# Kernel optimization log

Hardware: AMD Instinct MI355X
Metric: run time of the kernel (lower is better)

The kernel has to match this reference:

```python
import jax, jax.numpy as jnp
import numpy as np

EPS = 1e-5
SLOPE = 0.01  # LeakyReLU negative_slope

def _ln(x, g, b):
    m = jnp.mean(x, axis=-1, keepdims=True)
    v = jnp.mean((x - m) ** 2, axis=-1, keepdims=True)
    return (x - m) * jax.lax.rsqrt(v + EPS) * g + b

def _lrelu(x):
    return jnp.where(x >= 0, x, SLOPE * x)

def _s6(x, W1, b1, W2, b2, W3, b3, A):
    # x: (B, L, D); A: (D, N). Mamba-style S6 selective scan.
    Bm = x @ W2 + b2                       # (B, L, N) input-dependent B
    Cm = x @ W3 + b3                       # (B, L, N) input-dependent C
    delta = jax.nn.softplus(x @ W1 + b1)   # (B, L, D) step sizes
    dA = jnp.exp(jnp.einsum('bld,dn->bldn', delta, A))            # (B,L,D,N)
    dBx = jnp.einsum('bld,bln->bldn', delta, Bm) * x[..., None]    # (B,L,D,N) dB * x
    Bsz, L, D = x.shape
    N = A.shape[1]
    def step(h, inp):
        dA_t, dBx_t, C_t = inp
        h = dA_t * h + dBx_t                       # (B, D, N)
        return h, jnp.einsum('bn,bdn->bd', C_t, h)  # y_t: (B, D)
    xs = (jnp.transpose(dA, (1, 0, 2, 3)),
          jnp.transpose(dBx, (1, 0, 2, 3)),
          jnp.transpose(Cm, (1, 0, 2)))
    _, ys = jax.lax.scan(step, jnp.zeros((Bsz, D, N), x.dtype), xs)
    return jnp.transpose(ys, (1, 0, 2))  # (B, L, D)

def _fwd(text, audio, video, tW1, tb1, tg1, tbe1, tW2, tb2, tg2, tbe2, sW1, sb1, sW2, sb2, sW3, sb3, sA, aW1, ab1, ag1, abe1, aW2, ab2, ag2, abe2, vW1, vb1, vg1, vbe1, vW2, vb2, vg2, vbe2, cW1, cb1, cW2, cb2):
    # text branch: Linear+LN+LeakyReLU x2, Dropout(eval=identity), S6
    t = _lrelu(_ln(text @ tW1 + tb1, tg1, tbe1))
    t = _lrelu(_ln(t @ tW2 + tb2, tg2, tbe2))
    t = _s6(t, sW1, sb1, sW2, sb2, sW3, sb3, sA)
    # audio / video branches are computed but do not feed the output (as in source)
    a = _lrelu(_ln(audio @ aW1 + ab1, ag1, abe1))
    a = _lrelu(_ln(a @ aW2 + ab2, ag2, abe2))
    v = _lrelu(_ln(video @ vW1 + vb1, vg1, vbe1))
    v = _lrelu(_ln(v @ vW2 + vb2, vg2, vbe2))
    o1 = t @ cW1 + cb1
    return o1 @ cW2 + cb2  # (B, L, 2)

def setup_inputs() -> dict:
    key = jax.random.key(0)
    ks = iter(jax.random.split(key, 64))
    def W(shape, s=0.05):
        return jax.random.normal(next(ks), shape, jnp.float32) * s
    B, L = 64, 63
    d = {
        'text': jax.random.normal(next(ks), (B, L, 100), jnp.float32),
        'audio': jax.random.normal(next(ks), (B, L, 73), jnp.float32),
        'video': jax.random.normal(next(ks), (B, L, 100), jnp.float32),
        'tW1': W((100, 128)), 'tb1': jnp.zeros(128), 'tg1': jnp.ones(128), 'tbe1': jnp.zeros(128),
        'tW2': W((128, 100)), 'tb2': jnp.zeros(100), 'tg2': jnp.ones(100), 'tbe2': jnp.zeros(100),
        'sW1': W((100, 100)), 'sb1': jnp.zeros(100),
        'sW2': W((100, 300)), 'sb2': jnp.zeros(300),
        'sW3': W((100, 300)), 'sb3': jnp.zeros(300),
        'sA': jnp.full((100, 300), 1.0 / np.sqrt(300.0), jnp.float32),  # F.normalize(ones, dim=-1)
        'aW1': W((73, 256)), 'ab1': jnp.zeros(256), 'ag1': jnp.ones(256), 'abe1': jnp.zeros(256),
        'aW2': W((256, 100)), 'ab2': jnp.zeros(100), 'ag2': jnp.ones(100), 'abe2': jnp.zeros(100),
        'vW1': W((100, 256)), 'vb1': jnp.zeros(256), 'vg1': jnp.ones(256), 'vbe1': jnp.zeros(256),
        'vW2': W((256, 100)), 'vb2': jnp.zeros(100), 'vg2': jnp.ones(100), 'vbe2': jnp.zeros(100),
        'cW1': W((100, 50)), 'cb1': jnp.zeros(50),
        'cW2': W((50, 2)), 'cb2': jnp.zeros(2),
    }
    return d

def reference(text, audio, video, tW1, tb1, tg1, tbe1, tW2, tb2, tg2, tbe2, sW1, sb1, sW2, sb2, sW3, sb3, sA, aW1, ab1, ag1, abe1, aW2, ab2, ag2, abe2, vW1, vb1, vg1, vbe1, vW2, vb2, vg2, vbe2, cW1, cb1, cW2, cb2):
    return _fwd(text, audio, video, tW1, tb1, tg1, tbe1, tW2, tb2, tg2, tbe2, sW1, sb1, sW2, sb2, sW3, sb3, sA, aW1, ab1, ag1, abe1, aW2, ab2, ag2, abe2, vW1, vb1, vg1, vbe1, vW2, vb2, vg2, vbe2, cW1, cb1, cW2, cb2)
```

## Files before the change

kernel.cpp:

```cpp
#include <hip/hip_runtime.h>
#include <hip/hip_bf16.h>


typedef __hip_bfloat16 bf16;

#define BATCH 64
#define SEQ   63
#define ROWS  (BATCH * SEQ)
#define DIN   100
#define H1    128
#define DM    100
#define NS    300

__device__ __forceinline__ float2 up2(unsigned u) {
    float2 r;
    r.x = __uint_as_float(u << 16);
    r.y = __uint_as_float(u & 0xffff0000u);
    return r;
}
template<bool ISB>
__device__ __forceinline__ float LD(const void* p, int i) {
    if (ISB) return __bfloat162float(((const bf16*)p)[i]);
    else     return ((const float*)p)[i];
}
template<bool ISB>
__device__ __forceinline__ float2 LD2(const void* p, int i) {
    if (ISB) return up2(((const unsigned*)p)[i]);
    else     return ((const float2*)p)[i];
}
__device__ __forceinline__ float waveReduceSum(float v) {
#pragma unroll
    for (int off = 32; off > 0; off >>= 1) v += __shfl_xor(v, off, 64);
    return v;
}
__device__ __forceinline__ float4 waveReduceSum4(float4 v) {
#pragma unroll
    for (int off = 32; off > 0; off >>= 1) {
        const float a = __shfl_xor(v.x, off, 64);
        const float b = __shfl_xor(v.y, off, 64);
        const float c = __shfl_xor(v.z, off, 64);
        const float d = __shfl_xor(v.w, off, 64);
        v.x += a; v.y += b; v.z += c; v.w += d;
    }
    return v;
}
__device__ __forceinline__ float lrelu(float x) { return x >= 0.f ? x : 0.01f * x; }
__device__ __forceinline__ float softplusf(float x) {
    return (x > 20.f) ? x : log1pf(__expf(x));
}
__device__ __forceinline__ bool flags_uniform(const float* __restrict__ f) {
    bool u = true;
#pragma unroll
    for (int i = 0; i < 8; ++i) u &= (f[i] > 0.5f);
    return u;
}
__device__ __forceinline__ bool detect_bf16(const unsigned short* __restrict__ probe) {
    const int l = threadIdx.x & 63;
    const unsigned u0 = probe[l * 2];
    const unsigned u1 = probe[l * 2 + 1];
    const float v0 = fabsf(__uint_as_float(u0 << 16));
    const float v1 = fabsf(__uint_as_float(u1 << 16));
    const bool big = !(v0 < 1000.f) || !(v1 < 1000.f);
    const bool zero_even = (u0 == 0u);
    const unsigned long long mb = __ballot(big);
    const unsigned long long mz = __ballot(zero_even);
    return (mb == 0ULL) && (__popcll(mz) < 32);
}

template<bool ISB>
__device__ __forceinline__ void a_main(
    const void* __restrict__ text,
    const void* __restrict__ tW1, const void* __restrict__ tb1,
    const void* __restrict__ tg1, const void* __restrict__ tbe1,
    const void* __restrict__ tW2, const void* __restrict__ tb2,
    const void* __restrict__ tg2, const void* __restrict__ tbe2,
    const void* __restrict__ sW1w, const void* __restrict__ sb1,
    float* __restrict__ ddx, float* __restrict__ t2g,
    float* __restrict__ sW,
    float (&xb)[4][DIN][2], float (&t1b)[4][H1][2], float (&t2b)[4][DM][2])
{
    const int tid  = threadIdx.x;
    const int w    = tid >> 6;
    const int lane = tid & 63;
    const int r0   = blockIdx.x * 8 + w * 2;

    if (lane < 50) {
#pragma unroll
        for (int r = 0; r < 2; ++r) {
            const float2 xv = LD2<ISB>(text, (r0 + r) * 50 + lane);
            xb[w][2 * lane][r]     = xv.x;
            xb[w][2 * lane + 1][r] = xv.y;
        }
    }
    for (int i = tid; i < 6400; i += 256)
        *(float2*)&sW[2 * i] = LD2<ISB>(tW1, i);
    __syncthreads();

    const float2 b1v = LD2<ISB>(tb1, lane);
    float ax0 = b1v.x, ay0 = b1v.y, ax1 = b1v.x, ay1 = b1v.y;
#pragma unroll 10
    for (int k = 0; k < DIN; ++k) {
        const float2 wv = *(const float2*)&sW[k * 128 + 2 * lane];
        const float2 xv = *(const float2*)&xb[w][k][0];
        ax0 += xv.x * wv.x; ay0 += xv.x * wv.y;
        ax1 += xv.y * wv.x; ay1 += xv.y * wv.y;
    }
    {
        float4 red = waveReduceSum4(make_float4(
            ax0 + ay0, ax0 * ax0 + ay0 * ay0,
            ax1 + ay1, ax1 * ax1 + ay1 * ay1));
        const float m0 = red.x * (1.f / 128.f);
        const float rs0 = rsqrtf(red.y * (1.f / 128.f) - m0 * m0 + 1e-5f);
        const float m1 = red.z * (1.f / 128.f);
        const float rs1 = rsqrtf(red.w * (1.f / 128.f) - m1 * m1 + 1e-5f);
        const float2 g = LD2<ISB>(tg1, lane), be = LD2<ISB>(tbe1, lane);
        float2 v;
        v.x = lrelu((ax0 - m0) * rs0 * g.x + be.x);
        v.y = lrelu((ax1 - m1) * rs1 * g.x + be.x);
        *(float2*)&t1b[w][2 * lane][0] = v;
        v.x = lrelu((ay0 - m0) * rs0 * g.y + be.y);
        v.y = lrelu((ay1 - m1) * rs1 * g.y + be.y);
        *(float2*)&t1b[w][2 * lane + 1][0] = v;
    }
    __syncthreads();

    for (int i = tid; i < 6400; i += 256)
        *(float2*)&sW[2 * i] = LD2<ISB>(tW2, i);
    __syncthreads();

    const bool act = lane < 50;
    const int  li  = act ? lane : 0;
    const float2 b2v = LD2<ISB>(tb2, li);
    float cx0 = b2v.x, cy0 = b2v.y, cx1 = b2v.x, cy1 = b2v.y;
#pragma unroll 8
    for (int k = 0; k < H1; ++k) {
        const float2 wv = *(const float2*)&sW[k * 100 + 2 * li];
        const float2 tv = *(const float2*)&t1b[w][k][0];
        cx0 += tv.x * wv.x; cy0 += tv.x * wv.y;
        cx1 += tv.y * wv.x; cy1 += tv.y * wv.y;
    }
    float u0x, u0y, u1x, u1y;
    {
        float4 red = waveReduceSum4(act ? make_float4(
            cx0 + cy0, cx0 * cx0 + cy0 * cy0,
            cx1 + cy1, cx1 * cx1 + cy1 * cy1) : make_float4(0.f, 0.f, 0.f, 0.f));
        const float m0 = red.x * 0.01f;
        const float rs0 = rsqrtf(red.y * 0.01f - m0 * m0 + 1e-5f);
        const float m1 = red.z * 0.01f;
        const float rs1 = rsqrtf(red.w * 0.01f - m1 * m1 + 1e-5f);
        if (act) {
            const float2 g = LD2<ISB>(tg2, lane), be = LD2<ISB>(tbe2, lane);
            u0x = lrelu((cx0 - m0) * rs0 * g.x + be.x);
            u0y = lrelu((cy0 - m0) * rs0 * g.y + be.y);
            u1x = lrelu((cx1 - m1) * rs1 * g.x + be.x);
            u1y = lrelu((cy1 - m1) * rs1 * g.y + be.y);
            t2b[w][2 * lane][0] = u0x; t2b[w][2 * lane + 1][0] = u0y;
            t2b[w][2 * lane][1] = u1x; t2b[w][2 * lane + 1][1] = u1y;
            *(float2*)(t2g + (r0)     * DM + 2 * lane) = make_float2(u0x, u0y);
            *(float2*)(t2g + (r0 + 1) * DM + 2 * lane) = make_float2(u1x, u1y);
        }
    }
    __syncthreads();

    for (int i = tid; i < 5000; i += 256)
        *(float2*)&sW[2 * i] = LD2<ISB>(sW1w, i);
    __syncthreads();

    const float2 sbv = LD2<ISB>(sb1, li);
    float dA0x = sbv.x, dA0y = sbv.y, dA1x = sbv.x, dA1y = sbv.y;
#pragma unroll 10
    for (int k = 0; k < DM; ++k) {
        const float2 wv = *(const float2*)&sW[k * 100 + 2 * li];
        const float2 tv = *(const float2*)&t2b[w][k][0];
        dA0x += tv.x * wv.x; dA0y += tv.x * wv.y;
        dA1x += tv.y * wv.x; dA1y += tv.y * wv.y;
    }
    if (act) {
        float de0 = softplusf(dA0x), de1 = softplusf(dA0y);
        float4 o;
        o.x = de0; o.y = de0 * u0x; o.z = de1; o.w = de1 * u0y;
        *(float4*)(ddx + (r0) * (2 * DM) + 4 * lane) = o;
        de0 = softplusf(dA1x); de1 = softplusf(dA1y);
        o.x = de0; o.y = de0 * u1x; o.z = de1; o.w = de1 * u1y;
        *(float4*)(ddx + (r0 + 1) * (2 * DM) + 4 * lane) = o;
    }
}

template<bool ISB>
__device__ __forceinline__ void a_prep(
    const void* __restrict__ sW2, const void* __restrict__ sb2,
    const void* __restrict__ sW3, const void* __restrict__ sb3,
    float* __restrict__ M33p, float* __restrict__ k0w, float* __restrict__ sW,
    int d3)
{
    const int tid = threadIdx.x;
    const int w = tid >> 6, lane = tid & 63;
    float* W3row = sW;
    float* b2v   = sW + 320;
    float* b3v   = sW + 640;
    for (int i = tid; i < 300; i += 256) {
        W3row[i] = LD<ISB>(sW3, d3 * 300 + i);
        b2v[i]   = LD<ISB>(sb2, i);
        b3v[i]   = LD<ISB>(sb3, i);
    }
    __syncthreads();
    for (int g = 0; g < 6; ++g) {
        const int d2 = w * 25 + g * 4;
        float4 p = make_float4(0.f, 0.f, 0.f, 0.f);
#pragma unroll
        for (int rep = 0; rep < 5; ++rep) {
            const int n = lane + 64 * rep;
            if (n < 300) {
                const float w3 = W3row[n];
                p.x += LD<ISB>(sW2, (d2 + 0) * 300 + n) * w3;
                p.y += LD<ISB>(sW2, (d2 + 1) * 300 + n) * w3;
                p.z += LD<ISB>(sW2, (d2 + 2) * 300 + n) * w3;
                p.w += LD<ISB>(sW2, (d2 + 3) * 300 + n) * w3;
            }
        }
        p = waveReduceSum4(p);
        if (lane == 0) {
            M33p[d3 * 102 + d2 + 0] = p.x;
            M33p[d3 * 102 + d2 + 1] = p.y;
            M33p[d3 * 102 + d2 + 2] = p.z;
            M33p[d3 * 102 + d2 + 3] = p.w;
        }
    }
    {
        const int d2 = w * 25 + 24;
        float4 p = make_float4(0.f, 0.f, 0.f, 0.f);
#pragma unroll
        for (int rep = 0; rep < 5; ++rep) {
            const int n = lane + 64 * rep;
            if (n < 300) {
                p.x += LD<ISB>(sW2, d2 * 300 + n) * W3row[n];
                if (w == 0) p.y += W3row[n] * b2v[n];
                if (w == 1) p.y += LD<ISB>(sW2, d3 * 300 + n) * b3v[n];
                if (w == 2 && d3 == 0) p.y += b2v[n] * b3v[n];
            }
        }
        p = waveReduceSum4(p);
        if (lane == 0) {
            M33p[d3 * 102 + d2] = p.x;
            if (w == 0) M33p[d3 * 102 + 100] = p.y;
            if (w == 1) M33p[d3 * 102 + 101] = p.y;
            if (w == 2 && d3 == 0) k0w[0] = p.y;
        }
    }
}

template<bool ISB>
__device__ __forceinline__ void a_check(
    const void* __restrict__ sA, float* __restrict__ Afl,
    float* __restrict__ sW, int j)
{
    const int tid = threadIdx.x;
    const float a0 = LD<ISB>(sA, 0);
    bool ok = true;
    for (int i = j * 3750 + tid; i < (j + 1) * 3750; i += 256)
        ok &= (LD<ISB>(sA, i) == a0);
    if (tid == 0) sW[960] = 1.f;
    __syncthreads();
    if (!ok) sW[960] = 0.f;
    __syncthreads();
    if (tid == 0) Afl[j] = sW[960];
    if (j == 0 && tid == 1) Afl[8] = a0;
}

template<bool ISB>
__device__ __forceinline__ void a_mkv(
    const void* __restrict__ cW1, const void* __restrict__ cb1,
    const void* __restrict__ cW2, const void* __restrict__ cb2,
    float* __restrict__ Mkv)
{
    const int t = threadIdx.x;
    if (t < 200) {
        const int d = t >> 1, j = t & 1;
        float m = 0.f;
#pragma unroll 5
        for (int i = 0; i < 50; ++i)
            m += LD<ISB>(cW1, d * 50 + i) * LD<ISB>(cW2, 2 * i + j);
        Mkv[t] = m;
    } else if (t < 202) {
        const int j = t - 200;
        float kv = LD<ISB>(cb2, j);
#pragma unroll 5
        for (int i = 0; i < 50; ++i)
            kv += LD<ISB>(cb1, i) * LD<ISB>(cW2, 2 * i + j);
        Mkv[200 + j] = kv;
    }
}

__global__ __launch_bounds__(256) void k_A(
    const void* text,
    const void* tW1, const void* tb1, const void* tg1, const void* tbe1,
    const void* tW2, const void* tb2, const void* tg2, const void* tbe2,
    const void* sW1w, const void* sb1,
    const void* sW2, const void* sb2, const void* sW3, const void* sb3,
    const void* sA,
    const void* cW1, const void* cb1, const void* cW2, const void* cb2,
    float* ddx, float* t2g, float* Mkv, float* M33p, float* k0w, float* Afl,
    const unsigned short* probe)
{
    __shared__ __align__(16) float sW[12800];
    __shared__ __align__(16) float xb[4][DIN][2];
    __shared__ __align__(16) float t1b[4][H1][2];
    __shared__ __align__(16) float t2b[4][DM][2];
    const bool isb = detect_bf16(probe);
    const int blk = blockIdx.x;
    if (blk < 504) {
        if (isb) a_main<true >(text, tW1, tb1, tg1, tbe1, tW2, tb2, tg2, tbe2,
                               sW1w, sb1, ddx, t2g, sW, xb, t1b, t2b);
        else     a_main<false>(text, tW1, tb1, tg1, tbe1, tW2, tb2, tg2, tbe2,
                               sW1w, sb1, ddx, t2g, sW, xb, t1b, t2b);
    } else if (blk < 604) {
        if (isb) a_prep<true >(sW2, sb2, sW3, sb3, M33p, k0w, sW, blk - 504);
        else     a_prep<false>(sW2, sb2, sW3, sb3, M33p, k0w, sW, blk - 504);
    } else if (blk < 612) {
        if (isb) a_check<true >(sA, Afl, sW, blk - 604);
        else     a_check<false>(sA, Afl, sW, blk - 604);
    } else {
        if (isb) a_mkv<true >(cW1, cb1, cW2, cb2, Mkv);
        else     a_mkv<false>(cW1, cb1, cW2, cb2, Mkv);
    }
}

template<bool ISB>
__device__ __forceinline__ void gyh_impl(
    const float* __restrict__ t2g, const float* __restrict__ ddx,
    const float* __restrict__ M33p, const float* __restrict__ k0w,
    const float* __restrict__ Mkv, const float* __restrict__ Afl,
    void* __restrict__ outp,
    float* __restrict__ sT2, float* __restrict__ sM,
    float* __restrict__ sZ, float* __restrict__ sG,
    float* __restrict__ srv, float* __restrict__ sMk)
{
    const int bid = blockIdx.x;
    const int xcd = bid & 7;
    const int jj  = bid >> 3;
    const int b   = xcd * 8 + (jj >> 2);
    const int q   = jj & 3;
    const int tid = threadIdx.x;
    const int w = tid >> 6, lane = tid & 63;

    const int tmax  = (q * 16 + 15 < SEQ) ? q * 16 + 15 : SEQ - 1;
    const int srows = tmax + 1;

    float2 rdd[13];
#pragma unroll
    for (int j = 0; j < 13; ++j) {
        const int i = tid + j * 512;
        rdd[j] = (i < srows * 100) ? ((const float2*)ddx)[b * 6300 + i]
                                   : make_float2(0.f, 0.f);
    }

    for (int i = tid; i < srows * 50; i += 512) {
        const float2 v = ((const float2*)t2g)[b * 3150 + i];
        const int t = i / 50, k2 = i % 50;
        sT2[t * 102 + 2 * k2]     = v.x;
        sT2[t * 102 + 2 * k2 + 1] = v.y;
    }
    for (int i = tid; i < 5100; i += 512)
        *(float2*)&sM[2 * i] = ((const float2*)M33p)[i];
    if (tid < 202) sMk[tid] = Mkv[tid];
    __syncthreads();

    {
        const float mv0 = sM[lane * 102 + 101];
        const float mv1 = (lane < 36) ? sM[(64 + lane) * 102 + 101] : 0.f;
#pragma unroll
        for (int g = 0; g < 2; ++g) {
            float4 p;
            float acc[4];
#pragma unroll
            for (int i = 0; i < 4; ++i) {
                const int s = w * 8 + g * 4 + i;
                const int scl = (s <= tmax) ? s : 0;
                float a = sT2[scl * 102 + lane] * mv0;
                if (lane < 36) a += sT2[scl * 102 + 64 + lane] * mv1;
                acc[i] = a;
            }
            p = waveReduceSum4(make_float4(acc[0], acc[1], acc[2], acc[3]));
            if (lane == 0) {
                const int s0 = w * 8 + g * 4;
                srv[s0 + 0] = p.x; srv[s0 + 1] = p.y;
                srv[s0 + 2] = p.z; srv[s0 + 3] = p.w;
            }
        }
    }
    {
        const int l2 = (lane < 51) ? 2 * lane : 0;
        const int zr0 = w * 2, zr1 = w * 2 + 1;
        const int t0 = q * 16 + zr0;
        const int t1 = q * 16 + zr1;
        const int tc1 = (t1 <= tmax) ? t1 : tmax;
        float2 a0 = make_float2(0.f, 0.f);
        float2 a1 = make_float2(0.f, 0.f);
#pragma unroll 4
        for (int k = 0; k < 100; ++k) {
            const float2 wv = *(const float2*)&sM[k * 102 + l2];
            const float x0 = sT2[t0 * 102 + k];
            const float x1 = sT2[tc1 * 102 + k];
            a0.x += x0 * wv.x; a0.y += x0 * wv.y;
            a1.x += x1 * wv.x; a1.y += x1 * wv.y;
        }
        if (lane < 51) {
            *(float2*)&sZ[zr0 * 102 + l2] = a0;
            if (t1 <= tmax) *(float2*)&sZ[zr1 * 102 + l2] = a1;
        }
    }
    __syncthreads();

    {
        const float kz = k0w[0];
        const int sc  = (lane <= tmax) ? lane : tmax;
        const int zr0 = w * 2, zr1 = w * 2 + 1;
        const int t1  = q * 16 + zr1;
        float g0 = kz + sZ[zr0 * 102 + 100] + srv[sc];
        float g1 = kz + sZ[zr1 * 102 + 100] + srv[sc];
#pragma unroll 5
        for (int k2 = 0; k2 < 50; ++k2) {
            const float2 tv = *(const float2*)&sT2[sc * 102 + 2 * k2];
            const float2 z0 = *(const float2*)&sZ[zr0 * 102 + 2 * k2];
            const float2 z1 = *(const float2*)&sZ[zr1 * 102 + 2 * k2];
            g0 += z0.x * tv.x + z0.y * tv.y;
            g1 += z1.x * tv.x + z1.y * tv.y;
        }
        if (lane <= tmax) {
            sG[zr0 * 64 + lane] = g0;
            if (t1 <= tmax) sG[zr1 * 64 + lane] = g1;
        }
    }
    __syncthreads();

#pragma unroll
    for (int j = 0; j < 13; ++j) {
        const int i = tid + j * 512;
        if (i < srows * 100) {
            sT2[i] = rdd[j].x;
            sM[i]  = rdd[j].y;
        }
    }
    __syncthreads();

    {
        const float av = Afl[8];
        const int c = tid >> 7;
        const int d = tid & 127;
        const int L = (srows + 3) >> 2;
        const int s0 = c * L;
        const int s1 = (s0 + L < srows) ? s0 + L : srows;
        if (d < 100) {
            float Ts = 0.f;
            for (int s = s0; s < s1; ++s) Ts += sT2[s * 100 + d];
            sZ[c * 128 + d] = Ts;
        }
        __syncthreads();
        if (d < 100) {
            float D = 0.f;
            for (int cc = 0; cc < c; ++cc) D += sZ[cc * 128 + d];
            for (int s = s0; s < s1; ++s) {
                D += sT2[s * 100 + d];
                const float En = __expf(-av * D);
                sM[s * 100 + d] = sM[s * 100 + d] * En;
                const int zr = s - q * 16;
                if (zr >= 0) sM[6400 + zr * 100 + d] = __expf(av * D);
            }
        }
    }
    __syncthreads();

    {
        const int li = (lane < 50) ? lane : 49;
        const float4 mk = *(const float4*)&sMk[4 * li];
        float4 oc = make_float4(0.f, 0.f, 0.f, 0.f);
#pragma unroll
        for (int r = 0; r < 2; ++r) {
            const int zr = w * 2 + r;
            const int t  = q * 16 + zr;
            float o0 = 0.f, o1 = 0.f;
            if (t < SEQ) {
                float a0 = 0.f, a1 = 0.f;
                const int nf = (t + 1) >> 1;
                const float* gp = &sG[zr * 64];
                for (int s2 = 0; s2 < nf; ++s2) {
                    const float2 g2 = *(const float2*)&gp[2 * s2];
                    const float2 v0 = *(const float2*)&sM[(2 * s2) * 100 + 2 * li];
                    const float2 v1 = *(const float2*)&sM[(2 * s2 + 1) * 100 + 2 * li];
                    a0 += g2.x * v0.x + g2.y * v1.x;
                    a1 += g2.x * v0.y + g2.y * v1.y;
                }
                if ((t & 1) == 0) {
                    const float gg = gp[t];
                    const float2 vt = *(const float2*)&sM[t * 100 + 2 * li];
                    a0 += gg * vt.x; a1 += gg * vt.y;
                }
                const float2 e2 = *(const float2*)&sM[6400 + zr * 100 + 2 * li];
                const float y0 = (lane < 50) ? e2.x * a0 : 0.f;
                const float y1 = (lane < 50) ? e2.y * a1 : 0.f;
                o0 = y0 * mk.x + y1 * mk.z;
                o1 = y0 * mk.y + y1 * mk.w;
            }
            if (r == 0) { oc.x = o0; oc.y = o1; }
            else        { oc.z = o0; oc.w = o1; }
        }
        oc = waveReduceSum4(oc);
        if (lane == 0) {
            const float kv0 = sMk[200], kv1 = sMk[201];
#pragma unroll
            for (int r = 0; r < 2; ++r) {
                const int t = q * 16 + w * 2 + r;
                if (t >= SEQ) continue;
                const int row = b * SEQ + t;
                const float o0 = (r == 0 ? oc.x : oc.z) + kv0;
                const float o1 = (r == 0 ? oc.y : oc.w) + kv1;
                if (ISB) {
                    ((bf16*)outp)[row * 2 + 0] = __float2bfloat16(o0);
                    ((bf16*)outp)[row * 2 + 1] = __float2bfloat16(o1);
                } else {
                    *(float2*)((float*)outp + row * 2) = make_float2(o0, o1);
                }
            }
        }
    }
}

__global__ __launch_bounds__(512) void k_GYH(
    const float* __restrict__ t2g, const float* __restrict__ ddx,
    const float* __restrict__ M33p, const float* __restrict__ k0w,
    const float* __restrict__ Mkv, const float* __restrict__ Afl,
    void* __restrict__ outp, const unsigned short* __restrict__ probe)
{
    __shared__ __align__(16) float sT2[6426];
    __shared__ __align__(16) float sM[10240];
    __shared__ __align__(16) float sZ[1632];
    __shared__ __align__(16) float sG[1024];
    __shared__ __align__(16) float srv[64];
    __shared__ __align__(16) float sMk[204];
    if (!flags_uniform(Afl)) return;
    if (detect_bf16(probe))
        gyh_impl<true >(t2g, ddx, M33p, k0w, Mkv, Afl, outp, sT2, sM, sZ, sG, srv, sMk);
    else
        gyh_impl<false>(t2g, ddx, M33p, k0w, Mkv, Afl, outp, sT2, sM, sZ, sG, srv, sMk);
}

template<bool ISB>
__device__ __forceinline__ float4 LD4(const void* p, int i) {
    if (ISB) {
        const uint2 u = ((const uint2*)p)[i];
        float4 r;
        r.x = __uint_as_float(u.x << 16);
        r.y = __uint_as_float(u.x & 0xffff0000u);
        r.z = __uint_as_float(u.y << 16);
        r.w = __uint_as_float(u.y & 0xffff0000u);
        return r;
    } else return ((const float4*)p)[i];
}

template<bool ISB>
__device__ __forceinline__ void b_impl(
    const float* __restrict__ t2g,
    const void* __restrict__ sW2, const void* __restrict__ sb2,
    const void* __restrict__ sW3, const void* __restrict__ sb3,
    float* __restrict__ BC, float (&sT)[DM][8])
{
    const int t  = threadIdx.x;
    const int r0 = blockIdx.x * 8;
    if (t < DM) {
#pragma unroll
        for (int r = 0; r < 8; ++r) sT[t][r] = t2g[(r0 + r) * DM + t];
    }
    __syncthreads();
    const bool isB = t < 75;
    const bool valid = t < 150;
    const int colbase = isB ? 4 * t : (valid ? 4 * (t - 75) : 0);
    const void* Wp   = isB ? sW2 : sW3;
    const void* bias = isB ? sb2 : sb3;
    const int rs4 = NS >> 2;
    const int cb4 = colbase >> 2;
    float4 acc[8];
    {
        const float4 bv = LD4<ISB>(bias, cb4);
#pragma unroll
        for (int r = 0; r < 8; ++r) acc[r] = bv;
    }
    float4 ring[4];
#pragma unroll
    for (int j = 0; j < 4; ++j) ring[j] = LD4<ISB>(Wp, j * rs4 + cb4);
    for (int kk = 0; kk < DM; kk += 4) {
#pragma unroll
        for (int j = 0; j < 4; ++j) {
            const int k = kk + j;
            const float4 wv = ring[j];
            if (k + 4 < DM) ring[j] = LD4<ISB>(Wp, (k + 4) * rs4 + cb4);
            const float4 lo = *(const float4*)&sT[k][0];
            const float4 hi = *(const float4*)&sT[k][4];
            acc[0].x += lo.x * wv.x; acc[0].y += lo.x * wv.y; acc[0].z += lo.x * wv.z; acc[0].w += lo.x * wv.w;
            acc[1].x += lo.y * wv.x; acc[1].y += lo.y * wv.y; acc[1].z += lo.y * wv.z; acc[1].w += lo.y * wv.w;
            acc[2].x += lo.z * wv.x; acc[2].y += lo.z * wv.y; acc[2].z += lo.z * wv.z; acc[2].w += lo.z * wv.w;
            acc[3].x += lo.w * wv.x; acc[3].y += lo.w * wv.y; acc[3].z += lo.w * wv.z; acc[3].w += lo.w * wv.w;
            acc[4].x += hi.x * wv.x; acc[4].y += hi.x * wv.y; acc[4].z += hi.x * wv.z; acc[4].w += hi.x * wv.w;
            acc[5].x += hi.y * wv.x; acc[5].y += hi.y * wv.y; acc[5].z += hi.y * wv.z; acc[5].w += hi.y * wv.w;
            acc[6].x += hi.z * wv.x; acc[6].y += hi.z * wv.y; acc[6].z += hi.z * wv.z; acc[6].w += hi.z * wv.w;
            acc[7].x += hi.w * wv.x; acc[7].y += hi.w * wv.y; acc[7].z += hi.w * wv.z; acc[7].w += hi.w * wv.w;
        }
    }
    if (valid) {
        const int off = isB ? 0 : 1;
#pragma unroll
        for (int r = 0; r < 8; ++r) {
            float* bp = BC + (r0 + r) * (2 * NS) + 2 * colbase + off;
            bp[0] = acc[r].x; bp[2] = acc[r].y;
            bp[4] = acc[r].z; bp[6] = acc[r].w;
        }
    }
}

__global__ __launch_bounds__(192, 1) void k_B(
    const float* t2g, const void* sW2, const void* sb2,
    const void* sW3, const void* sb3, float* BC,
    const float* Afl, const unsigned short* probe)
{
    __shared__ __align__(16) float sT[DM][8];
    if (flags_uniform(Afl)) return;
    if (detect_bf16(probe)) b_impl<true >(t2g, sW2, sb2, sW3, sb3, BC, sT);
    else                    b_impl<false>(t2g, sW2, sb2, sW3, sb3, BC, sT);
}

template<bool ISB>
__device__ __forceinline__ void scan_impl(
    const float* __restrict__ ddx, const float* __restrict__ BC,
    const void* __restrict__ sA, float* __restrict__ y,
    float (&sacc)[4][16][2][68])
{
    const int w    = threadIdx.x >> 6;
    const int lane = threadIdx.x & 63;
    const int wid  = blockIdx.x * 4 + w;
    const int b    = wid / 50;
    const int dp   = wid % 50;
    const int d0   = 2 * dp, d1 = d0 + 1;

    int nc[5]; bool nv[5];
    float A0[5], A1[5], h0[5], h1[5];
#pragma unroll
    for (int c = 0; c < 5; ++c) {
        const int n = lane + 64 * c;
        nv[c] = n < NS;
        nc[c] = nv[c] ? n : 0;
        A0[c] = nv[c] ? LD<ISB>(sA, d0 * NS + nc[c]) : 0.f;
        A1[c] = nv[c] ? LD<ISB>(sA, d1 * NS + nc[c]) : 0.f;
        h0[c] = 0.f; h1[c] = 0.f;
    }
    const float* ddp = ddx + (b * SEQ) * (2 * DM) + 4 * dp;
    const float* BCp = BC  + (b * SEQ) * (2 * NS);
    float*       yp  = y   + (b * SEQ) * DM + d0;

    float4 pdd[3];
    float2 pbc[3][5];
#pragma unroll
    for (int j = 0; j < 3; ++j) {
        pdd[j] = *(const float4*)(ddp + j * (2 * DM));
#pragma unroll
        for (int c = 0; c < 5; ++c)
            pbc[j][c] = nv[c] ? *(const float2*)(BCp + j * (2 * NS) + 2 * nc[c])
                              : make_float2(0.f, 0.f);
    }
    const int pr = lane >> 1;
    const int hh = lane & 1;
    const int sa = pr & 15;
    const int aa = pr >> 4;

#pragma unroll 3
    for (int l = 0; l < SEQ; ++l) {
        const int bi = l % 3;
        const float4 dd = pdd[bi];
        float2 bc[5];
#pragma unroll
        for (int c = 0; c < 5; ++c) bc[c] = pbc[bi][c];
        if (l + 3 < SEQ) {
            pdd[bi] = *(const float4*)(ddp + (l + 3) * (2 * DM));
#pragma unroll
            for (int c = 0; c < 5; ++c)
                pbc[bi][c] = nv[c] ? *(const float2*)(BCp + (l + 3) * (2 * NS) + 2 * nc[c])
                                   : make_float2(0.f, 0.f);
        }
        float a0 = 0.f, a1 = 0.f;
#pragma unroll
        for (int c = 0; c < 5; ++c) {
            h0[c] = __expf(dd.x * A0[c]) * h0[c] + dd.y * bc[c].x;
            a0 += bc[c].y * h0[c];
            h1[c] = __expf(dd.z * A1[c]) * h1[c] + dd.w * bc[c].x;
            a1 += bc[c].y * h1[c];
        }
        const int s = l & 15;
        sacc[w][s][0][lane] = a0;
        sacc[w][s][1][lane] = a1;

        if (s == 15 || l == SEQ - 1) {
            const int l0 = l & ~15;
            const int cs = l - l0 + 1;
            float sum = 0.f;
            if (sa < cs) {
                const float* rowp = &sacc[w][sa][aa][hh * 32];
#pragma unroll
                for (int i = 0; i < 8; ++i) {
                    const float4 v = *(const float4*)(rowp + 4 * i);
                    sum += v.x + v.y + v.z + v.w;
                }
            }
            sum += __shfl_xor(sum, 1, 64);
            if (hh == 0 && sa < cs) yp[(l0 + sa) * DM + aa] = sum;
        }
    }
}

__global__ __launch_bounds__(256) void k_scan(
    const float* ddx, const float* BC, const void* sA, float* y,
    const float* Afl, const unsigned short* probe)
{
    __shared__ __align__(16) float sacc[4][16][2][68];
    if (flags_uniform(Afl)) return;
    if (detect_bf16(probe)) scan_impl<true >(ddx, BC, sA, y, sacc);
    else                    scan_impl<false>(ddx, BC, sA, y, sacc);
}

template<bool ISB>
__device__ __forceinline__ void headf_impl(
    const float* __restrict__ y, const float* __restrict__ Mkv,
    void* __restrict__ outp)
{
    const int row = blockIdx.x * 256 + threadIdx.x;
    if (row >= ROWS) return;
    float a0 = Mkv[200], a1 = Mkv[201];
    const float* yr = y + row * DM;
#pragma unroll 4
    for (int k = 0; k < DM; ++k) {
        const float v = yr[k];
        const float2 m = *(const float2*)(Mkv + 2 * k);
        a0 += v * m.x;
        a1 += v * m.y;
    }
    if (ISB) {
        ((bf16*)outp)[row * 2 + 0] = __float2bfloat16(a0);
        ((bf16*)outp)[row * 2 + 1] = __float2bfloat16(a1);
    } else {
        *(float2*)((float*)outp + row * 2) = make_float2(a0, a1);
    }
}

__global__ __launch_bounds__(256) void k_headF(
    const float* y, const float* Mkv, void* outp,
    const float* Afl, const unsigned short* probe)
{
    if (flags_uniform(Afl)) return;
    if (detect_bf16(probe)) headf_impl<true >(y, Mkv, outp);
    else                    headf_impl<false>(y, Mkv, outp);
}

extern "C" void kernel_launch(void* const* d_in, const int* in_sizes, int n_in,
                              void* d_out, int out_size, void* d_ws, size_t ws_size,
                              hipStream_t stream)
{
    const void* text = d_in[0];
    const void* tW1  = d_in[3];
    const void* tb1  = d_in[4];
    const void* tg1  = d_in[5];
    const void* tbe1 = d_in[6];
    const void* tW2  = d_in[7];
    const void* tb2  = d_in[8];
    const void* tg2  = d_in[9];
    const void* tbe2 = d_in[10];
    const void* sW1  = d_in[11];
    const void* sb1  = d_in[12];
    const void* sW2  = d_in[13];
    const void* sb2  = d_in[14];
    const void* sW3  = d_in[15];
    const void* sb3  = d_in[16];
    const void* sA   = d_in[17];
    const void* cW1  = d_in[34];
    const void* cb1  = d_in[35];
    const void* cW2  = d_in[36];
    const void* cb2  = d_in[37];
    const unsigned short* probe = (const unsigned short*)d_in[3];

    float* ws   = (float*)d_ws;
    float* ddx  = ws;
    float* BCv  = ddx + ROWS * 2 * DM;
    float* yv   = BCv + ROWS * 2 * NS;
    float* Mkv  = yv + ROWS * DM;
    float* M33p = Mkv + 202;
    float* k0w  = M33p + 10200;
    float* Afl  = k0w + 1;
    float* t2g  = yv;

    k_A<<<613, 256, 0, stream>>>(
        text, tW1, tb1, tg1, tbe1, tW2, tb2, tg2, tbe2,
        sW1, sb1, sW2, sb2, sW3, sb3, sA,
        cW1, cb1, cW2, cb2,
        ddx, t2g, Mkv, M33p, k0w, Afl, probe);

    k_GYH<<<BATCH * 4, 512, 0, stream>>>(t2g, ddx, M33p, k0w, Mkv, Afl,
                                         d_out, probe);

    k_B<<<ROWS / 8, 192, 0, stream>>>(t2g, sW2, sb2, sW3, sb3, BCv, Afl, probe);
    k_scan<<<3200 / 4, 256, 0, stream>>>(ddx, BCv, sA, yv, Afl, probe);
    k_headF<<<(ROWS + 255) / 256, 256, 0, stream>>>(yv, Mkv, d_out, Afl, probe);
}
```

Baseline: 175.1 us.

## Halve weight LDS tile in k_A and interleave time rows in k_GYH

k_A now stages each weight matrix into shared memory in two halves, splitting every matvec into two passes. This cuts the sW buffer from 12800 to 6400 floats so more blocks can be resident, at the cost of extra barriers. k_GYH reassigns output timesteps so each block takes a strided set (q + 4*zr) instead of a contiguous chunk of 16, which evens out the triangular work across blocks. It also pads the sT2 row stride from 102 to 103 to reduce LDS bank conflicts.

Measured after the change: 189.7 us. +8.3%, slower.

```diff
diff --git a/kernel.cpp b/kernel.cpp
--- a/kernel.cpp
+++ b/kernel.cpp
@@ -92,16 +92,27 @@
             xb[w][2 * lane + 1][r] = xv.y;
         }
     }
-    for (int i = tid; i < 6400; i += 256)
+    for (int i = tid; i < 3200; i += 256)
         *(float2*)&sW[2 * i] = LD2<ISB>(tW1, i);
     __syncthreads();
 
     const float2 b1v = LD2<ISB>(tb1, lane);
     float ax0 = b1v.x, ay0 = b1v.y, ax1 = b1v.x, ay1 = b1v.y;
 #pragma unroll 10
-    for (int k = 0; k < DIN; ++k) {
+    for (int k = 0; k < 50; ++k) {
         const float2 wv = *(const float2*)&sW[k * 128 + 2 * lane];
         const float2 xv = *(const float2*)&xb[w][k][0];
+        ax0 += xv.x * wv.x; ay0 += xv.x * wv.y;
+        ax1 += xv.y * wv.x; ay1 += xv.y * wv.y;
+    }
+    __syncthreads();
+    for (int i = tid; i < 3200; i += 256)
+        *(float2*)&sW[2 * i] = LD2<ISB>(tW1, 3200 + i);
+    __syncthreads();
+#pragma unroll 10
+    for (int k = 0; k < 50; ++k) {
+        const float2 wv = *(const float2*)&sW[k * 128 + 2 * lane];
+        const float2 xv = *(const float2*)&xb[w][k + 50][0];
         ax0 += xv.x * wv.x; ay0 += xv.x * wv.y;
         ax1 += xv.y * wv.x; ay1 += xv.y * wv.y;
     }
@@ -124,7 +135,7 @@
     }
     __syncthreads();
 
-    for (int i = tid; i < 6400; i += 256)
+    for (int i = tid; i < 3200; i += 256)
         *(float2*)&sW[2 * i] = LD2<ISB>(tW2, i);
     __syncthreads();
 
@@ -133,9 +144,20 @@
     const float2 b2v = LD2<ISB>(tb2, li);
     float cx0 = b2v.x, cy0 = b2v.y, cx1 = b2v.x, cy1 = b2v.y;
 #pragma unroll 8
-    for (int k = 0; k < H1; ++k) {
+    for (int k = 0; k < 64; ++k) {
         const float2 wv = *(const float2*)&sW[k * 100 + 2 * li];
         const float2 tv = *(const float2*)&t1b[w][k][0];
+        cx0 += tv.x * wv.x; cy0 += tv.x * wv.y;
+        cx1 += tv.y * wv.x; cy1 += tv.y * wv.y;
+    }
+    __syncthreads();
+    for (int i = tid; i < 3200; i += 256)
+        *(float2*)&sW[2 * i] = LD2<ISB>(tW2, 3200 + i);
+    __syncthreads();
+#pragma unroll 8
+    for (int k = 0; k < 64; ++k) {
+        const float2 wv = *(const float2*)&sW[k * 100 + 2 * li];
+        const float2 tv = *(const float2*)&t1b[w][k + 64][0];
         cx0 += tv.x * wv.x; cy0 += tv.x * wv.y;
         cx1 += tv.y * wv.x; cy1 += tv.y * wv.y;
     }
@@ -162,16 +184,27 @@
     }
     __syncthreads();
 
-    for (int i = tid; i < 5000; i += 256)
+    for (int i = tid; i < 2500; i += 256)
         *(float2*)&sW[2 * i] = LD2<ISB>(sW1w, i);
     __syncthreads();
 
     const float2 sbv = LD2<ISB>(sb1, li);
     float dA0x = sbv.x, dA0y = sbv.y, dA1x = sbv.x, dA1y = sbv.y;
 #pragma unroll 10
-    for (int k = 0; k < DM; ++k) {
+    for (int k = 0; k < 50; ++k) {
         const float2 wv = *(const float2*)&sW[k * 100 + 2 * li];
         const float2 tv = *(const float2*)&t2b[w][k][0];
+        dA0x += tv.x * wv.x; dA0y += tv.x * wv.y;
+        dA1x += tv.y * wv.x; dA1y += tv.y * wv.y;
+    }
+    __syncthreads();
+    for (int i = tid; i < 2500; i += 256)
+        *(float2*)&sW[2 * i] = LD2<ISB>(sW1w, 2500 + i);
+    __syncthreads();
+#pragma unroll 10
+    for (int k = 0; k < 50; ++k) {
+        const float2 wv = *(const float2*)&sW[k * 100 + 2 * li];
+        const float2 tv = *(const float2*)&t2b[w][k + 50][0];
         dA0x += tv.x * wv.x; dA0y += tv.x * wv.y;
         dA1x += tv.y * wv.x; dA1y += tv.y * wv.y;
     }
@@ -302,7 +335,7 @@
     float* ddx, float* t2g, float* Mkv, float* M33p, float* k0w, float* Afl,
     const unsigned short* probe)
 {
-    __shared__ __align__(16) float sW[12800];
+    __shared__ __align__(16) float sW[6400];
     __shared__ __align__(16) float xb[4][DIN][2];
     __shared__ __align__(16) float t1b[4][H1][2];
     __shared__ __align__(16) float t2b[4][DM][2];
@@ -343,7 +376,7 @@
     const int tid = threadIdx.x;
     const int w = tid >> 6, lane = tid & 63;
 
-    const int tmax  = (q * 16 + 15 < SEQ) ? q * 16 + 15 : SEQ - 1;
+    const int tmax  = (q + 60 < SEQ) ? q + 60 : q + 56;
     const int srows = tmax + 1;
 
     float2 rdd[13];
@@ -357,8 +390,8 @@
     for (int i = tid; i < srows * 50; i += 512) {
         const float2 v = ((const float2*)t2g)[b * 3150 + i];
         const int t = i / 50, k2 = i % 50;
-        sT2[t * 102 + 2 * k2]     = v.x;
-        sT2[t * 102 + 2 * k2 + 1] = v.y;
+        sT2[t * 103 + 2 * k2]     = v.x;
+        sT2[t * 103 + 2 * k2 + 1] = v.y;
     }
     for (int i = tid; i < 5100; i += 512)
         *(float2*)&sM[2 * i] = ((const float2*)M33p)[i];
@@ -376,8 +409,8 @@
             for (int i = 0; i < 4; ++i) {
                 const int s = w * 8 + g * 4 + i;
                 const int scl = (s <= tmax) ? s : 0;
-                float a = sT2[scl * 102 + lane] * mv0;
-                if (lane < 36) a += sT2[scl * 102 + 64 + lane] * mv1;
+                float a = sT2[scl * 103 + lane] * mv0;
+                if (lane < 36) a += sT2[scl * 103 + 64 + lane] * mv1;
                 acc[i] = a;
             }
             p = waveReduceSum4(make_float4(acc[0], acc[1], acc[2], acc[3]));
@@ -388,25 +421,27 @@
             }
         }
     }
+    const int zr0 = w;
+    const int zr1 = 15 - w;
+    const int t0  = q + 4 * zr0;
+    const int t1  = q + 4 * zr1;
+    const bool v1 = (t1 < SEQ);
     {
         const int l2 = (lane < 51) ? 2 * lane : 0;
-        const int zr0 = w * 2, zr1 = w * 2 + 1;
-        const int t0 = q * 16 + zr0;
-        const int t1 = q * 16 + zr1;
-        const int tc1 = (t1 <= tmax) ? t1 : tmax;
+        const int tc1 = v1 ? t1 : tmax;
         float2 a0 = make_float2(0.f, 0.f);
         float2 a1 = make_float2(0.f, 0.f);
 #pragma unroll 4
         for (int k = 0; k < 100; ++k) {
             const float2 wv = *(const float2*)&sM[k * 102 + l2];
-            const float x0 = sT2[t0 * 102 + k];
-            const float x1 = sT2[tc1 * 102 + k];
+            const float x0 = sT2[t0 * 103 + k];
+            const float x1 = sT2[tc1 * 103 + k];
             a0.x += x0 * wv.x; a0.y += x0 * wv.y;
             a1.x += x1 * wv.x; a1.y += x1 * wv.y;
         }
         if (lane < 51) {
             *(float2*)&sZ[zr0 * 102 + l2] = a0;
-            if (t1 <= tmax) *(float2*)&sZ[zr1 * 102 + l2] = a1;
+            if (v1) *(float2*)&sZ[zr1 * 102 + l2] = a1;
         }
     }
     __syncthreads();
@@ -414,13 +449,11 @@
     {
         const float kz = k0w[0];
         const int sc  = (lane <= tmax) ? lane : tmax;
-        const int zr0 = w * 2, zr1 = w * 2 + 1;
-        const int t1  = q * 16 + zr1;
         float g0 = kz + sZ[zr0 * 102 + 100] + srv[sc];
         float g1 = kz + sZ[zr1 * 102 + 100] + srv[sc];
 #pragma unroll 5
         for (int k2 = 0; k2 < 50; ++k2) {
-            const float2 tv = *(const float2*)&sT2[sc * 102 + 2 * k2];
+            const float2 tv = *(const float2*)&sT2[sc * 103 + 2 * k2];
             const float2 z0 = *(const float2*)&sZ[zr0 * 102 + 2 * k2];
             const float2 z1 = *(const float2*)&sZ[zr1 * 102 + 2 * k2];
             g0 += z0.x * tv.x + z0.y * tv.y;
@@ -428,7 +461,7 @@
         }
         if (lane <= tmax) {
             sG[zr0 * 64 + lane] = g0;
-            if (t1 <= tmax) sG[zr1 * 64 + lane] = g1;
+            if (v1) sG[zr1 * 64 + lane] = g1;
         }
     }
     __syncthreads();
@@ -463,8 +496,9 @@
                 D += sT2[s * 100 + d];
                 const float En = __expf(-av * D);
                 sM[s * 100 + d] = sM[s * 100 + d] * En;
-                const int zr = s - q * 16;
-                if (zr >= 0) sM[6400 + zr * 100 + d] = __expf(av * D);
+                const int sq = s - q;
+                if (sq >= 0 && (sq & 3) == 0)
+                    sM[6400 + (sq >> 2) * 100 + d] = __expf(av * D);
             }
         }
     }
@@ -476,8 +510,8 @@
         float4 oc = make_float4(0.f, 0.f, 0.f, 0.f);
 #pragma unroll
         for (int r = 0; r < 2; ++r) {
-            const int zr = w * 2 + r;
-            const int t  = q * 16 + zr;
+            const int zr = r ? zr1 : zr0;
+            const int t  = q + 4 * zr;
             float o0 = 0.f, o1 = 0.f;
             if (t < SEQ) {
                 float a0 = 0.f, a1 = 0.f;
@@ -486,9 +520,9 @@
                 for (int s2 = 0; s2 < nf; ++s2) {
                     const float2 g2 = *(const float2*)&gp[2 * s2];
                     const float2 v0 = *(const float2*)&sM[(2 * s2) * 100 + 2 * li];
-                    const float2 v1 = *(const float2*)&sM[(2 * s2 + 1) * 100 + 2 * li];
-                    a0 += g2.x * v0.x + g2.y * v1.x;
-                    a1 += g2.x * v0.y + g2.y * v1.y;
+                    const float2 v1v = *(const float2*)&sM[(2 * s2 + 1) * 100 + 2 * li];
+                    a0 += g2.x * v0.x + g2.y * v1v.x;
+                    a1 += g2.x * v0.y + g2.y * v1v.y;
                 }
                 if ((t & 1) == 0) {
                     const float gg = gp[t];
@@ -509,7 +543,7 @@
             const float kv0 = sMk[200], kv1 = sMk[201];
 #pragma unroll
             for (int r = 0; r < 2; ++r) {
-                const int t = q * 16 + w * 2 + r;
+                const int t = q + 4 * (r ? zr1 : zr0);
                 if (t >= SEQ) continue;
                 const int row = b * SEQ + t;
                 const float o0 = (r == 0 ? oc.x : oc.z) + kv0;
@@ -531,7 +565,7 @@
     const float* __restrict__ Mkv, const float* __restrict__ Afl,
     void* __restrict__ outp, const unsigned short* __restrict__ probe)
 {
-    __shared__ __align__(16) float sT2[6426];
+    __shared__ __align__(16) float sT2[6496];
     __shared__ __align__(16) float sM[10240];
     __shared__ __align__(16) float sZ[1632];
     __shared__ __align__(16) float sG[1024];
```
